# Kernel tuning notes

Measured on AMD Instinct MI355X. Metric: run time of the kernel, lower is better.

## Reference

```python
import jax, jax.numpy as jnp
import numpy as np

B, N, D, S, H, ITERS = 64, 4096, 128, 7, 256, 3
EPS = 1e-8

def layer_norm(x, g, b):
    m = jnp.mean(x, axis=-1, keepdims=True)
    v = jnp.var(x, axis=-1, keepdims=True)
    return (x - m) * jax.lax.rsqrt(v + 1e-5) * g + b

def setup_inputs() -> dict:
    key = jax.random.key(0)
    ks = jax.random.split(key, 16)
    lin = lambda k, o, i: jax.random.normal(k, (o, i), jnp.float32) / np.sqrt(i)
    return {
        "embeddings": jax.random.normal(ks[0], (B, N, D), jnp.float32),
        "noise": jax.random.normal(ks[1], (B, S, D), jnp.float32),
        "slots_mu": jax.random.normal(ks[2], (1, 1, D), jnp.float32),
        "slots_sigma": jax.random.uniform(ks[3], (1, 1, D), jnp.float32),
        "Wk": lin(ks[4], D, D), "bk": jnp.zeros((D,), jnp.float32),
        "Wq": lin(ks[5], D, D), "bq": jnp.zeros((D,), jnp.float32),
        "Wv": lin(ks[6], D, D), "bv": jnp.zeros((D,), jnp.float32),
        "W_ih": lin(ks[7], 3 * D, D), "W_hh": lin(ks[8], 3 * D, D),
        "b_ih": jnp.zeros((3 * D,), jnp.float32), "b_hh": jnp.zeros((3 * D,), jnp.float32),
        "W1": lin(ks[9], H, D), "b1": jnp.zeros((H,), jnp.float32),
        "W2": lin(ks[10], D, H), "b2": jnp.zeros((D,), jnp.float32),
        "ln_in_g": jnp.ones((D,), jnp.float32), "ln_in_b": jnp.zeros((D,), jnp.float32),
        "ln_s_g": jnp.ones((D,), jnp.float32), "ln_s_b": jnp.zeros((D,), jnp.float32),
        "ln_ff_g": jnp.ones((D,), jnp.float32), "ln_ff_b": jnp.zeros((D,), jnp.float32),
    }

def reference(embeddings, noise, slots_mu, slots_sigma, Wk, bk, Wq, bq, Wv, bv,
              W_ih, W_hh, b_ih, b_hh, W1, b1, W2, b2,
              ln_in_g, ln_in_b, ln_s_g, ln_s_b, ln_ff_g, ln_ff_b):
    # slot init: normal(mu, sigma) with fixed noise
    slots = slots_mu + slots_sigma * noise  # [B,S,D]
    emb = layer_norm(embeddings, ln_in_g, ln_in_b)
    keys = emb @ Wk.T + bk      # [B,N,D]
    values = emb @ Wv.T + bv    # [B,N,D]
    for _ in range(ITERS):
        slots_prev = slots
        q = layer_norm(slots, ln_s_g, ln_s_b) @ Wq.T + bq  # [B,S,D]
        dots = jnp.einsum('bid,bjd->bij', q, keys)          # [B,S,N]
        attn = jax.nn.softmax(dots, axis=-1) + EPS
        attn = attn / jnp.sum(attn, axis=-1, keepdims=True)
        updates = jnp.einsum('bjd,bij->bid', values, attn)  # [B,S,D]
        # GRUCell (pytorch gate order: r, z, n)
        x = updates.reshape(-1, D)
        h = slots_prev.reshape(-1, D)
        gi = x @ W_ih.T + b_ih
        gh = h @ W_hh.T + b_hh
        gi_r, gi_z, gi_n = jnp.split(gi, 3, axis=-1)
        gh_r, gh_z, gh_n = jnp.split(gh, 3, axis=-1)
        r = jax.nn.sigmoid(gi_r + gh_r)
        z = jax.nn.sigmoid(gi_z + gh_z)
        n = jnp.tanh(gi_n + r * gh_n)
        slots = ((1.0 - z) * n + z * h).reshape(B, S, D)
        ff = jax.nn.relu(layer_norm(slots, ln_ff_g, ln_ff_b) @ W1.T + b1) @ W2.T + b2
        slots = slots + ff
    return slots
```

## Files before the change

kernel.cpp:

```cpp
#include <hip/hip_runtime.h>
#include <math.h>

#define B_ 64
#define N_ 4096
#define D_ 128
#define S_ 7
#define H_ 256
#define ITERS_ 3
#define AP 132
#define NCHUNK 8

__device__ __forceinline__ float dot4(float4 a, float4 b) {
  return a.x * b.x + a.y * b.y + a.z * b.z + a.w * b.w;
}
__device__ __forceinline__ float4 ld4(const float* p) {
  return *reinterpret_cast<const float4*>(p);
}

__global__ void k_init(const float* __restrict__ noise, const float* __restrict__ mu,
                       const float* __restrict__ sigma, float* __restrict__ slots) {
  int idx = blockIdx.x * 256 + threadIdx.x;
  int d = idx & 127;
  slots[idx] = mu[d] + sigma[d] * noise[idx];
}

__global__ void k_wt(const float* __restrict__ W, float* __restrict__ out, int R, int C) {
  int idx = blockIdx.x * 256 + threadIdx.x;
  if (idx >= R * C) return;
  int d = idx / C, i = idx - d * C;
  out[(((i >> 2) * R + d) << 2) + (i & 3)] = W[idx];
}

__global__ __launch_bounds__(128) void k_q(
    const float* __restrict__ slots, const float* __restrict__ Wq, const float* __restrict__ bq,
    const float* __restrict__ g, const float* __restrict__ b,
    const float* __restrict__ Wk, float* __restrict__ qp) {
  __shared__ __align__(16) float lns[AP];
  __shared__ __align__(16) float qs2[AP];
  __shared__ float red[4];
  int row = blockIdx.x;
  int d = threadIdx.x;
  float x = slots[row * D_ + d];
  float s1 = x, s2 = x * x;
#pragma unroll
  for (int off = 32; off >= 1; off >>= 1) { s1 += __shfl_down(s1, off); s2 += __shfl_down(s2, off); }
  if ((d & 63) == 0) { red[(d >> 6) * 2] = s1; red[(d >> 6) * 2 + 1] = s2; }
  __syncthreads();
  float sum = red[0] + red[2], sumsq = red[1] + red[3];
  float mean = sum * (1.f / 128.f);
  float var = sumsq * (1.f / 128.f) - mean * mean;
  float rs = rsqrtf(var + 1e-5f);
  lns[d] = (x - mean) * rs * g[d] + b[d];
  __syncthreads();
  const float* w = Wq + d * D_;
  float acc = bq[d];
  for (int i4 = 0; i4 < D_; i4 += 4) acc += dot4(*reinterpret_cast<const float4*>(&lns[i4]), ld4(w + i4));
  qs2[d] = acc;
  __syncthreads();
  float qpa = 0.f;
#pragma unroll 4
  for (int dd = 0; dd < D_; dd++) qpa += qs2[dd] * Wk[dd * D_ + d];
  qp[row * D_ + d] = qpa;
}

__global__ __launch_bounds__(256) void k_attn(
    const float* __restrict__ qpbuf, const float* __restrict__ emb,
    const float* __restrict__ lng, const float* __restrict__ lnb,
    float* __restrict__ partialA, float* __restrict__ partialM, float* __restrict__ partialS) {
  __shared__ __align__(16) float lacc[16 * 7 * 128];
  __shared__ float lm[16 * 7], lsm[16 * 7];
  __shared__ float wgt[7 * 16];
  __shared__ float mstar[7];
  int t = threadIdx.x;
  int b = blockIdx.x >> 3, jc = blockIdx.x & (NCHUNK - 1);
  int lane = t & 63;
  int gid = (t >> 6) * 4 + (lane >> 4);
  int li = lane & 15;
  int i8 = li * 8;

  float4 q0[7], q1[7];
#pragma unroll
  for (int s = 0; s < 7; s++) {
    q0[s] = ld4(&qpbuf[(b * 7 + s) * D_ + i8]);
    q1[s] = ld4(&qpbuf[(b * 7 + s) * D_ + i8 + 4]);
  }
  float4 gv0 = ld4(&lng[i8]), gv1 = ld4(&lng[i8 + 4]);
  float4 bv0 = ld4(&lnb[i8]), bv1 = ld4(&lnb[i8 + 4]);

  float acc[7][8];
#pragma unroll
  for (int s = 0; s < 7; s++)
#pragma unroll
    for (int c = 0; c < 8; c++) acc[s][c] = 0.f;
  float m[7], ssum[7];
#pragma unroll
  for (int s = 0; s < 7; s++) { m[s] = -1e30f; ssum[s] = 0.f; }

  const float* src = emb + ((long)b * N_ + jc * 512 + gid * 32) * D_ + i8;
  float4 x0 = ld4(src), x1 = ld4(src + 4);
  for (int i = 0; i < 32; i++) {
    float4 c0 = x0, c1 = x1;
    if (i < 31) {
      x0 = ld4(src + (i + 1) * D_);
      x1 = ld4(src + (i + 1) * D_ + 4);
    }
    float s1 = c0.x + c0.y + c0.z + c0.w + c1.x + c1.y + c1.z + c1.w;
    float s2 = dot4(c0, c0) + dot4(c1, c1);
#pragma unroll
    for (int off = 8; off >= 1; off >>= 1) {
      s1 += __shfl_xor(s1, off, 16);
      s2 += __shfl_xor(s2, off, 16);
    }
    float mean = s1 * (1.f / 128.f);
    float var = s2 * (1.f / 128.f) - mean * mean;
    float rs = rsqrtf(var + 1e-5f);
    float4 o0, o1;
    o0.x = (c0.x - mean) * rs * gv0.x + bv0.x;
    o0.y = (c0.y - mean) * rs * gv0.y + bv0.y;
    o0.z = (c0.z - mean) * rs * gv0.z + bv0.z;
    o0.w = (c0.w - mean) * rs * gv0.w + bv0.w;
    o1.x = (c1.x - mean) * rs * gv1.x + bv1.x;
    o1.y = (c1.y - mean) * rs * gv1.y + bv1.y;
    o1.z = (c1.z - mean) * rs * gv1.z + bv1.z;
    o1.w = (c1.w - mean) * rs * gv1.w + bv1.w;
#pragma unroll
    for (int s = 0; s < 7; s++) {
      float p = dot4(o0, q0[s]) + dot4(o1, q1[s]);
#pragma unroll
      for (int off = 8; off >= 1; off >>= 1) p += __shfl_xor(p, off, 16);
      float mnew = fmaxf(m[s], p);
      float scl = __expf(m[s] - mnew);
      float e = __expf(p - mnew);
      m[s] = mnew;
      ssum[s] = ssum[s] * scl + e;
      acc[s][0] = acc[s][0] * scl + e * o0.x;
      acc[s][1] = acc[s][1] * scl + e * o0.y;
      acc[s][2] = acc[s][2] * scl + e * o0.z;
      acc[s][3] = acc[s][3] * scl + e * o0.w;
      acc[s][4] = acc[s][4] * scl + e * o1.x;
      acc[s][5] = acc[s][5] * scl + e * o1.y;
      acc[s][6] = acc[s][6] * scl + e * o1.z;
      acc[s][7] = acc[s][7] * scl + e * o1.w;
    }
  }

#pragma unroll
  for (int s = 0; s < 7; s++) {
    *reinterpret_cast<float4*>(&lacc[(gid * 7 + s) * 128 + i8]) =
        make_float4(acc[s][0], acc[s][1], acc[s][2], acc[s][3]);
    *reinterpret_cast<float4*>(&lacc[(gid * 7 + s) * 128 + i8 + 4]) =
        make_float4(acc[s][4], acc[s][5], acc[s][6], acc[s][7]);
  }
  if (li == 0) {
#pragma unroll
    for (int s = 0; s < 7; s++) { lm[gid * 7 + s] = m[s]; lsm[gid * 7 + s] = ssum[s]; }
  }
  __syncthreads();
  if (t < 7) {
    float mx = -1e30f;
#pragma unroll
    for (int g2 = 0; g2 < 16; g2++) mx = fmaxf(mx, lm[g2 * 7 + t]);
    mstar[t] = mx;
  }
  __syncthreads();
  if (t < 112) {
    int s = t >> 4, g2 = t & 15;
    wgt[s * 16 + g2] = __expf(lm[g2 * 7 + s] - mstar[s]);
  }
  __syncthreads();
  if (t < 7) {
    float dsum = 0.f;
#pragma unroll
    for (int g2 = 0; g2 < 16; g2++) dsum += wgt[t * 16 + g2] * lsm[g2 * 7 + t];
    partialM[(b * NCHUNK + jc) * 7 + t] = mstar[t];
    partialS[(b * NCHUNK + jc) * 7 + t] = dsum;
  }
  for (int pp = t; pp < 896; pp += 256) {
    int s = pp >> 7, d = pp & 127;
    float x = 0.f;
#pragma unroll
    for (int g2 = 0; g2 < 16; g2++) x += wgt[s * 16 + g2] * lacc[(g2 * 7 + s) * 128 + d];
    partialA[((long)(b * NCHUNK + jc) * 7 + s) * 128 + d] = x;
  }
}

__global__ __launch_bounds__(256) void k_gruffq(
    const float* __restrict__ partialA, const float* __restrict__ partialM,
    const float* __restrict__ partialS, float* __restrict__ slots,
    const float* __restrict__ wtV, const float* __restrict__ bv,
    const float* __restrict__ wtIH, const float* __restrict__ wtHH,
    const float* __restrict__ bih, const float* __restrict__ bhh,
    const float* __restrict__ wt1, const float* __restrict__ b1,
    const float* __restrict__ wt2, const float* __restrict__ b2,
    const float* __restrict__ gff, const float* __restrict__ bff,
    const float* __restrict__ lsg, const float* __restrict__ lsb,
    const float* __restrict__ wtQ, const float* __restrict__ bq,
    const float* __restrict__ Wk, float* __restrict__ qp, int compute_q) {
  __shared__ __align__(16) float us[AP];
  __shared__ __align__(16) float xs[AP];
  __shared__ __align__(16) float hs[AP];
  __shared__ __align__(16) float nss[AP];
  __shared__ __align__(16) float lns[AP];
  __shared__ __align__(16) float sn[AP];
  __shared__ __align__(16) float qv[AP];
  __shared__ __align__(16) float h1s[H_];
  __shared__ __align__(16) float g6[6 * 128];
  __shared__ __align__(16) float pp[2 * 128];
  __shared__ float den2[2];
  __shared__ float red2[2];
  int t = threadIdx.x;
  int d = t & 127, h = t >> 7;
  int blk = blockIdx.x;
  int b = blk / 7, s = blk % 7;

  float mg = -1e30f;
#pragma unroll
  for (int c = 0; c < NCHUNK; c++) mg = fmaxf(mg, partialM[(b * NCHUNK + c) * 7 + s]);
  float up = 0.f, den = 0.f;
#pragma unroll
  for (int cc = 0; cc < NCHUNK / 2; cc++) {
    int c = h * (NCHUNK / 2) + cc;
    float w = __expf(partialM[(b * NCHUNK + c) * 7 + s] - mg);
    den += w * partialS[(b * NCHUNK + c) * 7 + s];
    up += w * partialA[((long)(b * NCHUNK + c) * 7 + s) * 128 + d];
  }
  pp[h * 128 + d] = up;
  if (d == 0) den2[h] = den;
  if (h == 1) hs[d] = slots[blk * D_ + d];
  __syncthreads();
  if (h == 0) us[d] = (pp[d] + pp[128 + d]) / (den2[0] + den2[1]);
  __syncthreads();

  {
    float acc = 0.f;
#pragma unroll
    for (int k = 0; k < 16; k++) {
      int i4 = h * 16 + k;
      acc += dot4(*reinterpret_cast<const float4*>(&us[i4 * 4]),
                  ld4(wtV + (i4 * 128 + d) * 4));
    }
    pp[h * 128 + d] = acc;
  }
  __syncthreads();
  if (h == 0) xs[d] = bv[d] + pp[d] + pp[128 + d];
  __syncthreads();

  {
    const float* wt = (h == 0) ? wtIH : wtHH;
    const float* bias = (h == 0) ? bih : bhh;
    const float* vec = (h == 0) ? xs : hs;
    float a0 = bias[d], a1 = bias[128 + d], a2 = bias[256 + d];
#pragma unroll
    for (int i4 = 0; i4 < 32; i4++) {
      float4 v = *reinterpret_cast<const float4*>(&vec[i4 * 4]);
      a0 += dot4(v, ld4(wt + (i4 * 384 + d) * 4));
      a1 += dot4(v, ld4(wt + (i4 * 384 + 128 + d) * 4));
      a2 += dot4(v, ld4(wt + (i4 * 384 + 256 + d) * 4));
    }
    g6[(h * 3 + 0) * 128 + d] = a0;
    g6[(h * 3 + 1) * 128 + d] = a1;
    g6[(h * 3 + 2) * 128 + d] = a2;
  }
  __syncthreads();
  if (h == 0) {
    float gir = g6[d], giz = g6[128 + d], gin = g6[256 + d];
    float ghr = g6[384 + d], ghz = g6[512 + d], ghn = g6[640 + d];
    float r = 1.f / (1.f + __expf(-(gir + ghr)));
    float z = 1.f / (1.f + __expf(-(giz + ghz)));
    float n = tanhf(gin + r * ghn);
    nss[d] = (1.f - z) * n + z * hs[d];
  }
  __syncthreads();

  if (t < 64) {
    float v0 = nss[t], v1 = nss[t + 64];
    float s1 = v0 + v1, s2 = v0 * v0 + v1 * v1;
#pragma unroll
    for (int off = 32; off >= 1; off >>= 1) { s1 += __shfl_down(s1, off); s2 += __shfl_down(s2, off); }
    if (t == 0) { red2[0] = s1; red2[1] = s2; }
  }
  __syncthreads();
  {
    float mean = red2[0] * (1.f / 128.f);
    float var = red2[1] * (1.f / 128.f) - mean * mean;
    float rs = rsqrtf(var + 1e-5f);
    if (h == 0) lns[d] = (nss[d] - mean) * rs * gff[d] + bff[d];
  }
  __syncthreads();

  {
    float a = b1[t];
#pragma unroll
    for (int i4 = 0; i4 < 32; i4++)
      a += dot4(*reinterpret_cast<const float4*>(&lns[i4 * 4]),
                ld4(wt1 + (i4 * 256 + t) * 4));
    h1s[t] = fmaxf(a, 0.f);
  }
  __syncthreads();

  {
    float acc = 0.f;
#pragma unroll
    for (int k = 0; k < 32; k++) {
      int h4 = h * 32 + k;
      acc += dot4(*reinterpret_cast<const float4*>(&h1s[h4 * 4]),
                  ld4(wt2 + (h4 * 128 + d) * 4));
    }
    pp[h * 128 + d] = acc;
  }
  __syncthreads();
  if (h == 0) {
    float out = nss[d] + b2[d] + pp[d] + pp[128 + d];
    sn[d] = out;
    slots[blk * D_ + d] = out;
  }
  __syncthreads();

  if (!compute_q) return;

  if (t < 64) {
    float v0 = sn[t], v1 = sn[t + 64];
    float s1 = v0 + v1, s2 = v0 * v0 + v1 * v1;
#pragma unroll
    for (int off = 32; off >= 1; off >>= 1) { s1 += __shfl_down(s1, off); s2 += __shfl_down(s2, off); }
    if (t == 0) { red2[0] = s1; red2[1] = s2; }
  }
  __syncthreads();
  {
    float mean = red2[0] * (1.f / 128.f);
    float var = red2[1] * (1.f / 128.f) - mean * mean;
    float rs = rsqrtf(var + 1e-5f);
    if (h == 0) lns[d] = (sn[d] - mean) * rs * lsg[d] + lsb[d];
  }
  __syncthreads();
  {
    float acc = 0.f;
#pragma unroll
    for (int k = 0; k < 16; k++) {
      int i4 = h * 16 + k;
      acc += dot4(*reinterpret_cast<const float4*>(&lns[i4 * 4]),
                  ld4(wtQ + (i4 * 128 + d) * 4));
    }
    pp[h * 128 + d] = acc;
  }
  __syncthreads();
  if (h == 0) qv[d] = bq[d] + pp[d] + pp[128 + d];
  __syncthreads();
  {
    float acc = 0.f;
    const float* wc = Wk + h * 64 * D_ + d;
#pragma unroll 4
    for (int dd = 0; dd < 64; dd++) acc += qv[h * 64 + dd] * wc[dd * D_];
    pp[h * 128 + d] = acc;
  }
  __syncthreads();
  if (h == 0) qp[blk * D_ + d] = pp[d] + pp[128 + d];
}

extern "C" void kernel_launch(void* const* d_in, const int* in_sizes, int n_in,
                              void* d_out, int out_size, void* d_ws, size_t ws_size,
                              hipStream_t stream) {
  const float* emb   = (const float*)d_in[0];
  const float* noise = (const float*)d_in[1];
  const float* mu    = (const float*)d_in[2];
  const float* sigma = (const float*)d_in[3];
  const float* Wk = (const float*)d_in[4];  const float* bk = (const float*)d_in[5];
  const float* Wq = (const float*)d_in[6];  const float* bq = (const float*)d_in[7];
  const float* Wv = (const float*)d_in[8];  const float* bv = (const float*)d_in[9];
  const float* Wih = (const float*)d_in[10]; const float* Whh = (const float*)d_in[11];
  const float* bih = (const float*)d_in[12]; const float* bhh = (const float*)d_in[13];
  const float* W1 = (const float*)d_in[14];  const float* b1 = (const float*)d_in[15];
  const float* W2 = (const float*)d_in[16];  const float* b2 = (const float*)d_in[17];
  const float* lin_g = (const float*)d_in[18]; const float* lin_b = (const float*)d_in[19];
  const float* ls_g  = (const float*)d_in[20]; const float* ls_b  = (const float*)d_in[21];
  const float* lff_g = (const float*)d_in[22]; const float* lff_b = (const float*)d_in[23];
  (void)bk;

  float* slots = (float*)d_out;
  float* qp       = (float*)d_ws;
  float* partialA = qp + (size_t)B_ * S_ * D_;
  float* partialM = partialA + (size_t)B_ * NCHUNK * S_ * D_;
  float* partialS = partialM + (size_t)B_ * NCHUNK * S_;
  float* wtV  = partialS + (size_t)B_ * NCHUNK * S_;
  float* wtIH = wtV + 16384;
  float* wtHH = wtIH + 49152;
  float* wtQ  = wtHH + 49152;
  float* wt1  = wtQ + 16384;
  float* wt2  = wt1 + 32768;

  k_init<<<224, 256, 0, stream>>>(noise, mu, sigma, slots);
  k_wt<<<64, 256, 0, stream>>>(Wv, wtV, 128, 128);
  k_wt<<<192, 256, 0, stream>>>(Wih, wtIH, 384, 128);
  k_wt<<<192, 256, 0, stream>>>(Whh, wtHH, 384, 128);
  k_wt<<<64, 256, 0, stream>>>(Wq, wtQ, 128, 128);
  k_wt<<<128, 256, 0, stream>>>(W1, wt1, 256, 128);
  k_wt<<<128, 256, 0, stream>>>(W2, wt2, 128, 256);
  k_q<<<448, 128, 0, stream>>>(slots, Wq, bq, ls_g, ls_b, Wk, qp);
  for (int it = 0; it < ITERS_; it++) {
    k_attn<<<B_ * NCHUNK, 256, 0, stream>>>(qp, emb, lin_g, lin_b, partialA, partialM, partialS);
    k_gruffq<<<448, 256, 0, stream>>>(partialA, partialM, partialS, slots, wtV, bv,
                                      wtIH, wtHH, bih, bhh, wt1, b1, wt2, b2, lff_g, lff_b,
                                      ls_g, ls_b, wtQ, bq, Wk, qp, it < ITERS_ - 1 ? 1 : 0);
  }
}
```

Baseline: 444.5 us.

## Cache per-row layernorm stats, use lazy softmax rescaling, merge weight transposes

```diff
diff --git a/kernel.cpp b/kernel.cpp
--- a/kernel.cpp
+++ b/kernel.cpp
@@ -24,11 +24,23 @@
   slots[idx] = mu[d] + sigma[d] * noise[idx];
 }
 
-__global__ void k_wt(const float* __restrict__ W, float* __restrict__ out, int R, int C) {
+__global__ void k_wt_all(const float* __restrict__ Wv, const float* __restrict__ Wih,
+                         const float* __restrict__ Whh, const float* __restrict__ Wq,
+                         const float* __restrict__ W1, const float* __restrict__ W2,
+                         float* __restrict__ wtV, float* __restrict__ wtIH,
+                         float* __restrict__ wtHH, float* __restrict__ wtQ,
+                         float* __restrict__ wt1, float* __restrict__ wt2) {
   int idx = blockIdx.x * 256 + threadIdx.x;
-  if (idx >= R * C) return;
-  int d = idx / C, i = idx - d * C;
-  out[(((i >> 2) * R + d) << 2) + (i & 3)] = W[idx];
+  const float* W; float* out; int R, C, base;
+  if (idx < 16384)       { W = Wv;  out = wtV;  R = 128; C = 128; base = 0; }
+  else if (idx < 65536)  { W = Wih; out = wtIH; R = 384; C = 128; base = 16384; }
+  else if (idx < 114688) { W = Whh; out = wtHH; R = 384; C = 128; base = 65536; }
+  else if (idx < 131072) { W = Wq;  out = wtQ;  R = 128; C = 128; base = 114688; }
+  else if (idx < 163840) { W = W1;  out = wt1;  R = 256; C = 128; base = 131072; }
+  else                   { W = W2;  out = wt2;  R = 128; C = 256; base = 163840; }
+  int i2 = idx - base;
+  int d = i2 / C, i = i2 - d * C;
+  out[(((i >> 2) * R + d) << 2) + (i & 3)] = W[i2];
 }
 
 __global__ __launch_bounds__(128) void k_q(
@@ -66,7 +78,8 @@
 __global__ __launch_bounds__(256) void k_attn(
     const float* __restrict__ qpbuf, const float* __restrict__ emb,
     const float* __restrict__ lng, const float* __restrict__ lnb,
-    float* __restrict__ partialA, float* __restrict__ partialM, float* __restrict__ partialS) {
+    float* __restrict__ partialA, float* __restrict__ partialM, float* __restrict__ partialS,
+    float* __restrict__ rowstat, int stat_mode) {
   __shared__ __align__(16) float lacc[16 * 7 * 128];
   __shared__ float lm[16 * 7], lsm[16 * 7];
   __shared__ float wgt[7 * 16];
@@ -96,24 +109,35 @@
 #pragma unroll
   for (int s = 0; s < 7; s++) { m[s] = -1e30f; ssum[s] = 0.f; }
 
-  const float* src = emb + ((long)b * N_ + jc * 512 + gid * 32) * D_ + i8;
+  long rowbase = (long)b * N_ + jc * 512 + gid * 32;
+  const float* src = emb + rowbase * D_ + i8;
+  float2* stw = reinterpret_cast<float2*>(rowstat) + rowbase;
   float4 x0 = ld4(src), x1 = ld4(src + 4);
+  float2 st = stat_mode ? stw[0] : make_float2(0.f, 0.f);
   for (int i = 0; i < 32; i++) {
     float4 c0 = x0, c1 = x1;
+    float2 stc = st;
     if (i < 31) {
       x0 = ld4(src + (i + 1) * D_);
       x1 = ld4(src + (i + 1) * D_ + 4);
-    }
-    float s1 = c0.x + c0.y + c0.z + c0.w + c1.x + c1.y + c1.z + c1.w;
-    float s2 = dot4(c0, c0) + dot4(c1, c1);
-#pragma unroll
-    for (int off = 8; off >= 1; off >>= 1) {
-      s1 += __shfl_xor(s1, off, 16);
-      s2 += __shfl_xor(s2, off, 16);
-    }
-    float mean = s1 * (1.f / 128.f);
-    float var = s2 * (1.f / 128.f) - mean * mean;
-    float rs = rsqrtf(var + 1e-5f);
+      if (stat_mode) st = stw[i + 1];
+    }
+    float mean, rs;
+    if (!stat_mode) {
+      float s1 = c0.x + c0.y + c0.z + c0.w + c1.x + c1.y + c1.z + c1.w;
+      float s2 = dot4(c0, c0) + dot4(c1, c1);
+#pragma unroll
+      for (int off = 8; off >= 1; off >>= 1) {
+        s1 += __shfl_xor(s1, off, 16);
+        s2 += __shfl_xor(s2, off, 16);
+      }
+      mean = s1 * (1.f / 128.f);
+      float var = s2 * (1.f / 128.f) - mean * mean;
+      rs = rsqrtf(var + 1e-5f);
+      if (li == 0) stw[i] = make_float2(mean, rs);
+    } else {
+      mean = stc.x; rs = stc.y;
+    }
     float4 o0, o1;
     o0.x = (c0.x - mean) * rs * gv0.x + bv0.x;
     o0.y = (c0.y - mean) * rs * gv0.y + bv0.y;
@@ -128,19 +152,23 @@
       float p = dot4(o0, q0[s]) + dot4(o1, q1[s]);
 #pragma unroll
       for (int off = 8; off >= 1; off >>= 1) p += __shfl_xor(p, off, 16);
-      float mnew = fmaxf(m[s], p);
-      float scl = __expf(m[s] - mnew);
-      float e = __expf(p - mnew);
-      m[s] = mnew;
-      ssum[s] = ssum[s] * scl + e;
-      acc[s][0] = acc[s][0] * scl + e * o0.x;
-      acc[s][1] = acc[s][1] * scl + e * o0.y;
-      acc[s][2] = acc[s][2] * scl + e * o0.z;
-      acc[s][3] = acc[s][3] * scl + e * o0.w;
-      acc[s][4] = acc[s][4] * scl + e * o1.x;
-      acc[s][5] = acc[s][5] * scl + e * o1.y;
-      acc[s][6] = acc[s][6] * scl + e * o1.z;
-      acc[s][7] = acc[s][7] * scl + e * o1.w;
+      if (p - m[s] > 8.f) {
+        float scl = __expf(m[s] - p);
+        ssum[s] *= scl;
+#pragma unroll
+        for (int c = 0; c < 8; c++) acc[s][c] *= scl;
+        m[s] = p;
+      }
+      float e = __expf(p - m[s]);
+      ssum[s] += e;
+      acc[s][0] += e * o0.x;
+      acc[s][1] += e * o0.y;
+      acc[s][2] += e * o0.z;
+      acc[s][3] += e * o0.w;
+      acc[s][4] += e * o1.x;
+      acc[s][5] += e * o1.y;
+      acc[s][6] += e * o1.z;
+      acc[s][7] += e * o1.w;
     }
   }
 
@@ -387,17 +415,16 @@
   float* wtQ  = wtHH + 49152;
   float* wt1  = wtQ + 16384;
   float* wt2  = wt1 + 32768;
+  float* rowstat = wt2 + 32768;
 
   k_init<<<224, 256, 0, stream>>>(noise, mu, sigma, slots);
-  k_wt<<<64, 256, 0, stream>>>(Wv, wtV, 128, 128);
-  k_wt<<<192, 256, 0, stream>>>(Wih, wtIH, 384, 128);
-  k_wt<<<192, 256, 0, stream>>>(Whh, wtHH, 384, 128);
-  k_wt<<<64, 256, 0, stream>>>(Wq, wtQ, 128, 128);
-  k_wt<<<128, 256, 0, stream>>>(W1, wt1, 256, 128);
-  k_wt<<<128, 256, 0, stream>>>(W2, wt2, 128, 256);
+  k_wt_all<<<768, 256, 0, stream>>>(Wv, Wih, Whh, Wq, W1, W2,
+                                    wtV, wtIH, wtHH, wtQ, wt1, wt2);
   k_q<<<448, 128, 0, stream>>>(slots, Wq, bq, ls_g, ls_b, Wk, qp);
   for (int it = 0; it < ITERS_; it++) {
-    k_attn<<<B_ * NCHUNK, 256, 0, stream>>>(qp, emb, lin_g, lin_b, partialA, partialM, partialS);
+    k_attn<<<B_ * NCHUNK, 256, 0, stream>>>(qp, emb, lin_g, lin_b,
+                                            partialA, partialM, partialS,
+                                            rowstat, it == 0 ? 0 : 1);
     k_gruffq<<<448, 256, 0, stream>>>(partialA, partialM, partialS, slots, wtV, bv,
                                       wtIH, wtHH, bih, bhh, wt1, b1, wt2, b2, lff_g, lff_b,
                                       ls_g, ls_b, wtQ, bq, Wk, qp, it < ITERS_ - 1 ? 1 : 0);
```

Measured after the change: 452.0 us. Within noise of the previous version (+1.7%).
